# Performance work log

Hardware: AMD Instinct MI355X
Metric: run time of the kernel (lower is better)

Reference implementation:

```python
import jax, jax.numpy as jnp
import numpy as np

N = 100000
IN_C, HID_C, OUT_C = 128, 128, 128
E = 3200000


def gcn_conv(x, src, dst, W, b, num_nodes):
    # Linear transform first (smaller feature dim already), then normalized scatter-add.
    h = x @ W  # [N, out]
    # symmetric normalization with self-loops already included in (src, dst)
    deg = jax.ops.segment_sum(jnp.ones_like(dst, dtype=h.dtype), dst, num_segments=num_nodes)
    dinv = jnp.where(deg > 0, jax.lax.rsqrt(deg), 0.0)  # deg^{-1/2}
    norm = dinv[src] * dinv[dst]  # [E_total]
    msgs = h[src] * norm[:, None]  # gather + scale, [E_total, out]
    out = jax.ops.segment_sum(msgs, dst, num_segments=num_nodes)  # scatter-add
    return out + b


def add_self_loops(edge_index, num_nodes):
    loop = jnp.arange(num_nodes, dtype=edge_index.dtype)
    src = jnp.concatenate([edge_index[0], loop])
    dst = jnp.concatenate([edge_index[1], loop])
    return src, dst


def setup_inputs() -> dict:
    key = jax.random.key(0)
    k1, k2, k3, k4, k5 = jax.random.split(key, 5)
    x = jax.random.normal(k1, (N, IN_C), dtype=jnp.float32)
    edge_index = jax.random.randint(k2, (2, E), 0, N, dtype=jnp.int64)
    # Glorot-ish init for GCN weights
    W1 = jax.random.normal(k3, (IN_C, HID_C), dtype=jnp.float32) * (1.0 / np.sqrt(IN_C))
    b1 = jnp.zeros((HID_C,), dtype=jnp.float32)
    W2 = jax.random.normal(k4, (HID_C, OUT_C), dtype=jnp.float32) * (1.0 / np.sqrt(HID_C))
    b2 = jnp.zeros((OUT_C,), dtype=jnp.float32)
    return {"x": x, "edge_index": edge_index, "W1": W1, "b1": b1, "W2": W2, "b2": b2}


def reference(x, edge_index, W1, b1, W2, b2):
    src, dst = add_self_loops(edge_index, N)
    h = gcn_conv(x, src, dst, W1, b1, N)
    h = jax.nn.relu(h)
    out = gcn_conv(h, src, dst, W2, b2, N)
    return out
```

## Files before the change

### kernel.cpp

```cpp
#include <hip/hip_runtime.h>


#define NPB 128
#define NBMAX 1024
#define EPT 64
#define PART_TILE (256 * EPT)
#define CAP 5120

typedef unsigned short ushort_t;
typedef unsigned long long ull_t;
typedef __attribute__((ext_vector_type(8))) short short8;
typedef __attribute__((ext_vector_type(4))) float f32x4;

__device__ __forceinline__ unsigned short f32_to_bf16_rne(float x) {
    unsigned int v = __float_as_uint(x);
    unsigned int r = v + 0x7fffu + ((v >> 16) & 1u);
    return (unsigned short)(r >> 16);
}

__global__ __launch_bounds__(256) void k_part2(
    const int* __restrict__ src, const int* __restrict__ dst,
    int* __restrict__ cnt, unsigned int* __restrict__ pairs,
    int e, int nbp, int total) {
    __shared__ int lcnt[NBMAX];
    __shared__ int lbase[NBMAX];
    int t = threadIdx.x;
    int t0 = blockIdx.x * PART_TILE;
    for (int k = t; k < nbp; k += 256) lcnt[k] = 0;
    __syncthreads();
#pragma unroll 4
    for (int j = 0; j < EPT; j++) {
        int i = t0 + j * 256 + t;
        if (i < total) {
            int d = (i < e) ? dst[i] : (i - e);
            atomicAdd(&lcnt[d >> 7], 1);
        }
    }
    __syncthreads();
    for (int k = t; k < nbp; k += 256) {
        int c = lcnt[k];
        lbase[k] = c ? atomicAdd(&cnt[k], c) : 0;
        lcnt[k] = 0;
    }
    __syncthreads();
#pragma unroll 4
    for (int j = 0; j < EPT; j++) {
        int i = t0 + j * 256 + t;
        if (i < total) {
            int s, d;
            if (i < e) { s = src[i]; d = dst[i]; }
            else       { s = i - e;  d = s; }
            int b = d >> 7;
            int off = atomicAdd(&lcnt[b], 1) + lbase[b];
            pairs[(size_t)b * CAP + off] =
                (unsigned int)s | ((unsigned int)(d & 127) << 17);
        }
    }
}

__global__ __launch_bounds__(256) void k_bscan(
    const int* __restrict__ cnt, int* __restrict__ bucket_ptr,
    int nbp, int total,
    const float* __restrict__ W1, const float* __restrict__ W2,
    ushort_t* __restrict__ Wp1, ushort_t* __restrict__ Wp2) {
    if (blockIdx.x > 0) {
        int idx = (blockIdx.x - 1) * 256 + threadIdx.x;
        int which = idx >> 14;
        int e = idx & 16383;
        int n = e & 127, k = e >> 7;
        const float* W = which ? W2 : W1;
        ushort_t* Wp = which ? Wp2 : Wp1;
        Wp[n * 128 + k] = f32_to_bf16_rne(W[k * 128 + n]);
        return;
    }
    __shared__ int sd[256];
    int t = threadIdx.x;
    int c[4];
#pragma unroll
    for (int j = 0; j < 4; j++) {
        int k = t * 4 + j;
        c[j] = (k < nbp) ? cnt[k] : 0;
    }
    int s = c[0] + c[1] + c[2] + c[3];
    sd[t] = s;
    __syncthreads();
    for (int off = 1; off < 256; off <<= 1) {
        int v = (t >= off) ? sd[t - off] : 0;
        __syncthreads();
        sd[t] += v;
        __syncthreads();
    }
    int pre = sd[t] - s;
#pragma unroll
    for (int j = 0; j < 4; j++) {
        int k = t * 4 + j;
        if (k < nbp) bucket_ptr[k] = pre;
        pre += c[j];
    }
    if (t == 255) bucket_ptr[nbp] = total;
}

__global__ __launch_bounds__(256) void k_build(
    const unsigned int* __restrict__ pairs, const int* __restrict__ cntg,
    const int* __restrict__ bucket_ptr,
    int* __restrict__ row_ptr, int* __restrict__ srcs,
    float* __restrict__ dinv, int n) {
    __shared__ int cnt[NPB];
    __shared__ int scn[NPB];
    __shared__ int cur[NPB];
    int b = blockIdx.x;
    int t = threadIdx.x;
    int node0 = b << 7;
    int cb = cntg[b];
    int p0 = bucket_ptr[b];
    const unsigned int* bp = pairs + (size_t)b * CAP;
    if (t < NPB) cnt[t] = 0;
    __syncthreads();
    for (int i = t; i < cb; i += 256) {
        int dlow = (int)(bp[i] >> 17) & 127;
        atomicAdd(&cnt[dlow], 1);
    }
    __syncthreads();
    if (t < NPB) scn[t] = cnt[t];
    __syncthreads();
    for (int off = 1; off < NPB; off <<= 1) {
        int v = (t < NPB && t >= off) ? scn[t - off] : 0;
        __syncthreads();
        if (t < NPB) scn[t] += v;
        __syncthreads();
    }
    if (t < NPB) {
        int incl = scn[t];
        int excl = incl - cnt[t];
        int start = p0 + excl;
        cur[t] = start;
        int node = node0 + t;
        if (node < n) {
            row_ptr[node] = start;
            dinv[node] = rsqrtf((float)cnt[t]);
            if (node == n - 1) row_ptr[n] = p0 + incl;
        }
    }
    __syncthreads();
    for (int i = t; i < cb; i += 256) {
        unsigned int pr = bp[i];
        int pos = atomicAdd(&cur[(pr >> 17) & 127], 1);
        srcs[pos] = (int)(pr & 0x1FFFFu);
    }
}

__global__ __launch_bounds__(256) void k_gemm1(
    const float* __restrict__ A, const ushort_t* __restrict__ Wp,
    const float* __restrict__ dinv, ushort_t* __restrict__ G, int M) {
    int t = threadIdx.x;
    int row0 = blockIdx.x * 64;
    int wv = t >> 6;
    int lane = t & 63;
    int m = lane & 15;
    int quad = lane >> 4;

    int gr_row = row0 + wv * 16 + m;
    int gcl = gr_row < M ? gr_row : M - 1;
    const float* ap = A + (size_t)gcl * 128 + quad * 8;

    f32x4 acc[8];
#pragma unroll
    for (int c = 0; c < 8; c++) acc[c] = (f32x4){0.f, 0.f, 0.f, 0.f};

#pragma unroll
    for (int ks = 0; ks < 4; ks++) {
        int kb = ks * 32 + quad * 8;
        float xs[8];
        *(float4*)&xs[0] = *(const float4*)(ap + ks * 32);
        *(float4*)&xs[4] = *(const float4*)(ap + ks * 32 + 4);
        short8 ahi, alo;
#pragma unroll
        for (int j = 0; j < 8; j++) {
            unsigned short h = f32_to_bf16_rne(xs[j]);
            ahi[j] = (short)h;
            float hf = __uint_as_float((unsigned int)h << 16);
            alo[j] = (short)f32_to_bf16_rne(xs[j] - hf);
        }
#pragma unroll
        for (int c = 0; c < 8; c++) {
            short8 b8 = *(const short8*)(Wp + (size_t)(c * 16 + m) * 128 + kb);
            acc[c] = __builtin_amdgcn_mfma_f32_16x16x32_bf16(ahi, b8, acc[c], 0, 0, 0);
            acc[c] = __builtin_amdgcn_mfma_f32_16x16x32_bf16(alo, b8, acc[c], 0, 0, 0);
        }
    }

    int rbase = row0 + wv * 16 + quad * 4;
#pragma unroll
    for (int reg = 0; reg < 4; reg++) {
        int gr = rbase + reg;
        if (gr < M) {
            float dv = dinv[gr];
#pragma unroll
            for (int c = 0; c < 8; c++)
                G[((size_t)(c >> 2) * M + gr) * 64 + (c & 3) * 16 + m] =
                    f32_to_bf16_rne(acc[c][reg] * dv);
        }
    }
}

__global__ __launch_bounds__(256) void k_gemm2(
    ushort_t* actG2, const ushort_t* __restrict__ Wp,
    const float* __restrict__ dinv, int M) {
    int t = threadIdx.x;
    int row0 = blockIdx.x * 64;
    int wv = t >> 6;
    int lane = t & 63;
    int m = lane & 15;
    int quad = lane >> 4;

    int gr_row = row0 + wv * 16 + m;
    int gcl = gr_row < M ? gr_row : M - 1;

    f32x4 acc[8];
#pragma unroll
    for (int c = 0; c < 8; c++) acc[c] = (f32x4){0.f, 0.f, 0.f, 0.f};

#pragma unroll
    for (int ks = 0; ks < 4; ks++) {
        int kb = ks * 32 + quad * 8;
        short8 a8 = *(const short8*)(actG2 + ((size_t)(kb >> 6) * M + gcl) * 64 + (kb & 63));
#pragma unroll
        for (int c = 0; c < 8; c++) {
            short8 b8 = *(const short8*)(Wp + (size_t)(c * 16 + m) * 128 + kb);
            acc[c] = __builtin_amdgcn_mfma_f32_16x16x32_bf16(a8, b8, acc[c], 0, 0, 0);
        }
    }

    int rbase = row0 + wv * 16 + quad * 4;
#pragma unroll
    for (int reg = 0; reg < 4; reg++) {
        int gr = rbase + reg;
        if (gr < M) {
            float dv = dinv[gr];
#pragma unroll
            for (int c = 0; c < 8; c++)
                actG2[((size_t)(c >> 2) * M + gr) * 64 + (c & 3) * 16 + m] =
                    f32_to_bf16_rne(acc[c][reg] * dv);
        }
    }
}


#define ACC_U(u)                                     \
    do {                                             \
        unsigned int ul_ = (unsigned int)(u);        \
        unsigned int uh_ = (unsigned int)((u) >> 32);\
        a0 += __uint_as_float(ul_ << 16);            \
        a1 += __uint_as_float(ul_ & 0xffff0000u);    \
        a2 += __uint_as_float(uh_ << 16);            \
        a3 += __uint_as_float(uh_ & 0xffff0000u);    \
    } while (0)

__global__ __launch_bounds__(256) void k_agg1(
    const int* __restrict__ row_ptr, const int* __restrict__ srcs,
    const ushort_t* __restrict__ G, const float* __restrict__ dinv,
    const float* __restrict__ bias, ull_t* __restrict__ ActOut,
    int n) {
    int bx = blockIdx.x;
    int chunk = bx & 1;
    int tile = bx >> 1;
    int t = threadIdx.x;
    int lane = t & 63;
    int g = lane >> 4;
    int q = lane & 15;
    int node = tile * 16 + (t >> 6) * 4 + g;
    bool valid = node < n;
    int nc = valid ? node : n - 1;
    int beg = row_ptr[nc], end = row_ptr[nc + 1];
    const ull_t* Tq = (const ull_t*)G + (size_t)chunk * n * 16 + q;
    float a0 = 0.f, a1 = 0.f, a2 = 0.f, a3 = 0.f;
    int e = beg;
    for (; e + 4 <= end; e += 4) {
        int s0 = srcs[e], s1 = srcs[e + 1], s2 = srcs[e + 2], s3 = srcs[e + 3];
        ull_t u0 = Tq[(size_t)s0 * 16];
        ull_t u1 = Tq[(size_t)s1 * 16];
        ull_t u2 = Tq[(size_t)s2 * 16];
        ull_t u3 = Tq[(size_t)s3 * 16];
        ACC_U(u0); ACC_U(u1); ACC_U(u2); ACC_U(u3);
    }
    for (; e < end; ++e) {
        int s = srcs[e];
        ull_t u = Tq[(size_t)s * 16];
        ACC_U(u);
    }
    if (valid) {
        float dv = dinv[node];
        const float* bp = bias + chunk * 64 + q * 4;
        a0 = fmaxf(fmaf(a0, dv, bp[0]), 0.f);
        a1 = fmaxf(fmaf(a1, dv, bp[1]), 0.f);
        a2 = fmaxf(fmaf(a2, dv, bp[2]), 0.f);
        a3 = fmaxf(fmaf(a3, dv, bp[3]), 0.f);
        unsigned int p0 = (unsigned int)f32_to_bf16_rne(a0) |
                          ((unsigned int)f32_to_bf16_rne(a1) << 16);
        unsigned int p1 = (unsigned int)f32_to_bf16_rne(a2) |
                          ((unsigned int)f32_to_bf16_rne(a3) << 16);
        ull_t uo = (ull_t)p0 | ((ull_t)p1 << 32);
        __builtin_nontemporal_store(uo, ActOut + ((size_t)chunk * n + node) * 16 + q);
    }
}

__global__ __launch_bounds__(256) void k_agg2(
    const int* __restrict__ row_ptr, const int* __restrict__ srcs,
    const ushort_t* __restrict__ G, const float* __restrict__ dinv,
    const float* __restrict__ bias, float* __restrict__ Out,
    int n) {
    int bx = blockIdx.x;
    int chunk = bx & 1;
    int tile = bx >> 1;
    int t = threadIdx.x;
    int lane = t & 63;
    int g = lane >> 4;
    int q = lane & 15;
    int node = tile * 16 + (t >> 6) * 4 + g;
    bool valid = node < n;
    int nc = valid ? node : n - 1;
    int beg = row_ptr[nc], end = row_ptr[nc + 1];
    const ull_t* Tq = (const ull_t*)G + (size_t)chunk * n * 16 + q;
    float a0 = 0.f, a1 = 0.f, a2 = 0.f, a3 = 0.f;
    int e = beg;
    for (; e + 4 <= end; e += 4) {
        int s0 = srcs[e], s1 = srcs[e + 1], s2 = srcs[e + 2], s3 = srcs[e + 3];
        ull_t u0 = Tq[(size_t)s0 * 16];
        ull_t u1 = Tq[(size_t)s1 * 16];
        ull_t u2 = Tq[(size_t)s2 * 16];
        ull_t u3 = Tq[(size_t)s3 * 16];
        ACC_U(u0); ACC_U(u1); ACC_U(u2); ACC_U(u3);
    }
    for (; e < end; ++e) {
        int s = srcs[e];
        ull_t u = Tq[(size_t)s * 16];
        ACC_U(u);
    }
    if (valid) {
        float dv = dinv[node];
        const float* bp = bias + chunk * 64 + q * 4;
        f32x4 o;
        o.x = fmaf(a0, dv, bp[0]);
        o.y = fmaf(a1, dv, bp[1]);
        o.z = fmaf(a2, dv, bp[2]);
        o.w = fmaf(a3, dv, bp[3]);
        __builtin_nontemporal_store(o,
            (f32x4*)(Out + (size_t)node * 128 + chunk * 64 + q * 4));
    }
}

extern "C" void kernel_launch(void* const* d_in, const int* in_sizes, int n_in,
                              void* d_out, int out_size, void* d_ws, size_t ws_size,
                              hipStream_t stream) {
    const float* x  = (const float*)d_in[0];
    const int*   ei = (const int*)d_in[1];
    const float* W1 = (const float*)d_in[2];
    const float* b1 = (const float*)d_in[3];
    const float* W2 = (const float*)d_in[4];
    const float* b2 = (const float*)d_in[5];
    float* out = (float*)d_out;

    const int C = 128;
    const int N = in_sizes[0] / C;
    const int E = in_sizes[1] / 2;
    const int* src = ei;
    const int* dst = ei + E;
    const int total = E + N;
    const int nbp = (N + NPB - 1) >> 7;
    const int T = (total + PART_TILE - 1) / PART_TILE;

    char* ws = (char*)d_ws;
    size_t off = 0;
    auto alloc = [&](size_t bytes) -> void* {
        void* p = ws + off;
        off = (off + bytes + 511) & ~(size_t)511;
        return p;
    };
    int*   cnt        = (int*)alloc((size_t)nbp * 4);
    int*   bucket_ptr = (int*)alloc((size_t)(nbp + 1) * 4);
    int*   row_ptr    = (int*)alloc(((size_t)N + 1) * 4);
    float* dinv       = (float*)alloc((size_t)N * 4);
    int*   srcs       = (int*)alloc((size_t)total * 4);
    ushort_t* Wp1     = (ushort_t*)alloc(128 * 128 * 2);
    ushort_t* Wp2     = (ushort_t*)alloc(128 * 128 * 2);
    ushort_t* G1      = (ushort_t*)alloc((size_t)N * C * 2);
    size_t ab = (size_t)N * C * 2, pb = (size_t)nbp * CAP * 4;
    void* shared = alloc(ab > pb ? ab : pb);
    ushort_t* actG2 = (ushort_t*)shared;
    unsigned int* pairs = (unsigned int*)shared;

    hipMemsetAsync(cnt, 0, (size_t)nbp * 4, stream);
    k_part2<<<T, 256, 0, stream>>>(src, dst, cnt, pairs, E, nbp, total);
    k_bscan<<<129, 256, 0, stream>>>(cnt, bucket_ptr, nbp, total,
                                     W1, W2, Wp1, Wp2);
    k_build<<<nbp, 256, 0, stream>>>(pairs, cnt, bucket_ptr,
                                     row_ptr, srcs, dinv, N);

    const int half = (N + 15) / 16;
    dim3 agrid(half * 2);

    k_gemm1<<<(N + 63) / 64, 256, 0, stream>>>(x, Wp1, dinv, G1, N);
    k_agg1<<<agrid, 256, 0, stream>>>(row_ptr, srcs, G1, dinv, b1,
                                      (ull_t*)actG2, N);

    k_gemm2<<<(N + 63) / 64, 256, 0, stream>>>(actG2, Wp2, dinv, N);
    k_agg2<<<agrid, 256, 0, stream>>>(row_ptr, srcs, actG2, dinv, b2, out, N);
}
```

Before: 496.0 us.

## Drop bucket scan kernel by using padded per-bucket CSR with start/end pairs

Removes the bucket prefix-scan kernel. Each bucket's sources are now stored at a fixed CAP-strided offset, and each node keeps a packed 64-bit start/end pair in place of row_ptr. The weight transpose and bf16 conversion moves into extra blocks of the partition kernel. The partition kernel now uses smaller tiles and keeps src/dst in registers, so edges are read once instead of twice. The aggregation kernels use nontemporal loads for the index streams. In exchange, srcs becomes a padded array and the partition launches more blocks with more global atomics.

```diff
diff --git a/kernel.cpp b/kernel.cpp
--- a/kernel.cpp
+++ b/kernel.cpp
@@ -3,8 +3,8 @@
 
 #define NPB 128
 #define NBMAX 1024
-#define EPT 64
-#define PART_TILE (256 * EPT)
+#define EPT2 16
+#define PART_TILE2 (256 * EPT2)
 #define CAP 5120
 
 typedef unsigned short ushort_t;
@@ -21,19 +21,36 @@
 __global__ __launch_bounds__(256) void k_part2(
     const int* __restrict__ src, const int* __restrict__ dst,
     int* __restrict__ cnt, unsigned int* __restrict__ pairs,
-    int e, int nbp, int total) {
+    int e, int nbp, int total, int T2,
+    const float* __restrict__ W1, const float* __restrict__ W2,
+    ushort_t* __restrict__ Wp1, ushort_t* __restrict__ Wp2) {
+    int blk = blockIdx.x;
+    int t = threadIdx.x;
+    if (blk >= T2) {
+        int idx = (blk - T2) * 256 + t;
+        int which = idx >> 14;
+        int ee = idx & 16383;
+        int n = ee & 127, k = ee >> 7;
+        const float* W = which ? W2 : W1;
+        ushort_t* Wp = which ? Wp2 : Wp1;
+        Wp[n * 128 + k] = f32_to_bf16_rne(W[k * 128 + n]);
+        return;
+    }
     __shared__ int lcnt[NBMAX];
     __shared__ int lbase[NBMAX];
-    int t = threadIdx.x;
-    int t0 = blockIdx.x * PART_TILE;
+    int t0 = blk * PART_TILE2;
     for (int k = t; k < nbp; k += 256) lcnt[k] = 0;
     __syncthreads();
-#pragma unroll 4
-    for (int j = 0; j < EPT; j++) {
+    int sv[EPT2], dvv[EPT2];
+#pragma unroll
+    for (int j = 0; j < EPT2; j++) {
         int i = t0 + j * 256 + t;
         if (i < total) {
-            int d = (i < e) ? dst[i] : (i - e);
-            atomicAdd(&lcnt[d >> 7], 1);
+            if (i < e) { sv[j] = src[i]; dvv[j] = dst[i]; }
+            else       { sv[j] = i - e;  dvv[j] = sv[j]; }
+            atomicAdd(&lcnt[dvv[j] >> 7], 1);
+        } else {
+            dvv[j] = -1;
         }
     }
     __syncthreads();
@@ -43,67 +60,20 @@
         lcnt[k] = 0;
     }
     __syncthreads();
-#pragma unroll 4
-    for (int j = 0; j < EPT; j++) {
-        int i = t0 + j * 256 + t;
-        if (i < total) {
-            int s, d;
-            if (i < e) { s = src[i]; d = dst[i]; }
-            else       { s = i - e;  d = s; }
-            int b = d >> 7;
+#pragma unroll
+    for (int j = 0; j < EPT2; j++) {
+        if (dvv[j] >= 0) {
+            int b = dvv[j] >> 7;
             int off = atomicAdd(&lcnt[b], 1) + lbase[b];
             pairs[(size_t)b * CAP + off] =
-                (unsigned int)s | ((unsigned int)(d & 127) << 17);
-        }
-    }
-}
-
-__global__ __launch_bounds__(256) void k_bscan(
-    const int* __restrict__ cnt, int* __restrict__ bucket_ptr,
-    int nbp, int total,
-    const float* __restrict__ W1, const float* __restrict__ W2,
-    ushort_t* __restrict__ Wp1, ushort_t* __restrict__ Wp2) {
-    if (blockIdx.x > 0) {
-        int idx = (blockIdx.x - 1) * 256 + threadIdx.x;
-        int which = idx >> 14;
-        int e = idx & 16383;
-        int n = e & 127, k = e >> 7;
-        const float* W = which ? W2 : W1;
-        ushort_t* Wp = which ? Wp2 : Wp1;
-        Wp[n * 128 + k] = f32_to_bf16_rne(W[k * 128 + n]);
-        return;
-    }
-    __shared__ int sd[256];
-    int t = threadIdx.x;
-    int c[4];
-#pragma unroll
-    for (int j = 0; j < 4; j++) {
-        int k = t * 4 + j;
-        c[j] = (k < nbp) ? cnt[k] : 0;
-    }
-    int s = c[0] + c[1] + c[2] + c[3];
-    sd[t] = s;
-    __syncthreads();
-    for (int off = 1; off < 256; off <<= 1) {
-        int v = (t >= off) ? sd[t - off] : 0;
-        __syncthreads();
-        sd[t] += v;
-        __syncthreads();
-    }
-    int pre = sd[t] - s;
-#pragma unroll
-    for (int j = 0; j < 4; j++) {
-        int k = t * 4 + j;
-        if (k < nbp) bucket_ptr[k] = pre;
-        pre += c[j];
-    }
-    if (t == 255) bucket_ptr[nbp] = total;
+                (unsigned int)sv[j] | ((unsigned int)(dvv[j] & 127) << 17);
+        }
+    }
 }
 
 __global__ __launch_bounds__(256) void k_build(
     const unsigned int* __restrict__ pairs, const int* __restrict__ cntg,
-    const int* __restrict__ bucket_ptr,
-    int* __restrict__ row_ptr, int* __restrict__ srcs,
+    ull_t* __restrict__ row_se, int* __restrict__ srcs,
     float* __restrict__ dinv, int n) {
     __shared__ int cnt[NPB];
     __shared__ int scn[NPB];
@@ -112,8 +82,8 @@
     int t = threadIdx.x;
     int node0 = b << 7;
     int cb = cntg[b];
-    int p0 = bucket_ptr[b];
-    const unsigned int* bp = pairs + (size_t)b * CAP;
+    int base = b * CAP;
+    const unsigned int* bp = pairs + (size_t)base;
     if (t < NPB) cnt[t] = 0;
     __syncthreads();
     for (int i = t; i < cb; i += 256) {
@@ -132,20 +102,20 @@
     if (t < NPB) {
         int incl = scn[t];
         int excl = incl - cnt[t];
-        int start = p0 + excl;
-        cur[t] = start;
+        cur[t] = excl;
         int node = node0 + t;
         if (node < n) {
-            row_ptr[node] = start;
+            row_se[node] = (ull_t)(unsigned int)(base + excl) |
+                           ((ull_t)(unsigned int)(base + incl) << 32);
             dinv[node] = rsqrtf((float)cnt[t]);
-            if (node == n - 1) row_ptr[n] = p0 + incl;
-        }
-    }
-    __syncthreads();
+        }
+    }
+    __syncthreads();
+    int* bs = srcs + (size_t)base;
     for (int i = t; i < cb; i += 256) {
         unsigned int pr = bp[i];
         int pos = atomicAdd(&cur[(pr >> 17) & 127], 1);
-        srcs[pos] = (int)(pr & 0x1FFFFu);
+        bs[pos] = (int)(pr & 0x1FFFFu);
     }
 }
 
@@ -257,7 +227,7 @@
     } while (0)
 
 __global__ __launch_bounds__(256) void k_agg1(
-    const int* __restrict__ row_ptr, const int* __restrict__ srcs,
+    const ull_t* __restrict__ row_se, const int* __restrict__ srcs,
     const ushort_t* __restrict__ G, const float* __restrict__ dinv,
     const float* __restrict__ bias, ull_t* __restrict__ ActOut,
     int n) {
@@ -271,12 +241,16 @@
     int node = tile * 16 + (t >> 6) * 4 + g;
     bool valid = node < n;
     int nc = valid ? node : n - 1;
-    int beg = row_ptr[nc], end = row_ptr[nc + 1];
+    ull_t se = __builtin_nontemporal_load(&row_se[nc]);
+    int beg = (int)(unsigned int)se, end = (int)(unsigned int)(se >> 32);
     const ull_t* Tq = (const ull_t*)G + (size_t)chunk * n * 16 + q;
     float a0 = 0.f, a1 = 0.f, a2 = 0.f, a3 = 0.f;
     int e = beg;
     for (; e + 4 <= end; e += 4) {
-        int s0 = srcs[e], s1 = srcs[e + 1], s2 = srcs[e + 2], s3 = srcs[e + 3];
+        int s0 = __builtin_nontemporal_load(&srcs[e]);
+        int s1 = __builtin_nontemporal_load(&srcs[e + 1]);
+        int s2 = __builtin_nontemporal_load(&srcs[e + 2]);
+        int s3 = __builtin_nontemporal_load(&srcs[e + 3]);
         ull_t u0 = Tq[(size_t)s0 * 16];
         ull_t u1 = Tq[(size_t)s1 * 16];
         ull_t u2 = Tq[(size_t)s2 * 16];
@@ -284,7 +258,7 @@
         ACC_U(u0); ACC_U(u1); ACC_U(u2); ACC_U(u3);
     }
     for (; e < end; ++e) {
-        int s = srcs[e];
+        int s = __builtin_nontemporal_load(&srcs[e]);
         ull_t u = Tq[(size_t)s * 16];
         ACC_U(u);
     }
@@ -305,7 +279,7 @@
 }
 
 __global__ __launch_bounds__(256) void k_agg2(
-    const int* __restrict__ row_ptr, const int* __restrict__ srcs,
+    const ull_t* __restrict__ row_se, const int* __restrict__ srcs,
     const ushort_t* __restrict__ G, const float* __restrict__ dinv,
     const float* __restrict__ bias, float* __restrict__ Out,
     int n) {
@@ -319,12 +293,16 @@
     int node = tile * 16 + (t >> 6) * 4 + g;
     bool valid = node < n;
     int nc = valid ? node : n - 1;
-    int beg = row_ptr[nc], end = row_ptr[nc + 1];
+    ull_t se = __builtin_nontemporal_load(&row_se[nc]);
+    int beg = (int)(unsigned int)se, end = (int)(unsigned int)(se >> 32);
     const ull_t* Tq = (const ull_t*)G + (size_t)chunk * n * 16 + q;
     float a0 = 0.f, a1 = 0.f, a2 = 0.f, a3 = 0.f;
     int e = beg;
     for (; e + 4 <= end; e += 4) {
-        int s0 = srcs[e], s1 = srcs[e + 1], s2 = srcs[e + 2], s3 = srcs[e + 3];
+        int s0 = __builtin_nontemporal_load(&srcs[e]);
+        int s1 = __builtin_nontemporal_load(&srcs[e + 1]);
+        int s2 = __builtin_nontemporal_load(&srcs[e + 2]);
+        int s3 = __builtin_nontemporal_load(&srcs[e + 3]);
         ull_t u0 = Tq[(size_t)s0 * 16];
         ull_t u1 = Tq[(size_t)s1 * 16];
         ull_t u2 = Tq[(size_t)s2 * 16];
@@ -332,7 +310,7 @@
         ACC_U(u0); ACC_U(u1); ACC_U(u2); ACC_U(u3);
     }
     for (; e < end; ++e) {
-        int s = srcs[e];
+        int s = __builtin_nontemporal_load(&srcs[e]);
         ull_t u = Tq[(size_t)s * 16];
         ACC_U(u);
     }
@@ -367,7 +345,7 @@
     const int* dst = ei + E;
     const int total = E + N;
     const int nbp = (N + NPB - 1) >> 7;
-    const int T = (total + PART_TILE - 1) / PART_TILE;
+    const int T2 = (total + PART_TILE2 - 1) / PART_TILE2;
 
     char* ws = (char*)d_ws;
     size_t off = 0;
@@ -376,33 +354,30 @@
         off = (off + bytes + 511) & ~(size_t)511;
         return p;
     };
-    int*   cnt        = (int*)alloc((size_t)nbp * 4);
-    int*   bucket_ptr = (int*)alloc((size_t)(nbp + 1) * 4);
-    int*   row_ptr    = (int*)alloc(((size_t)N + 1) * 4);
-    float* dinv       = (float*)alloc((size_t)N * 4);
-    int*   srcs       = (int*)alloc((size_t)total * 4);
-    ushort_t* Wp1     = (ushort_t*)alloc(128 * 128 * 2);
-    ushort_t* Wp2     = (ushort_t*)alloc(128 * 128 * 2);
-    ushort_t* G1      = (ushort_t*)alloc((size_t)N * C * 2);
+    int*   cnt     = (int*)alloc((size_t)nbp * 4);
+    ull_t* row_se  = (ull_t*)alloc((size_t)N * 8);
+    float* dinv    = (float*)alloc((size_t)N * 4);
+    int*   srcs    = (int*)alloc((size_t)nbp * CAP * 4);
+    ushort_t* Wp1  = (ushort_t*)alloc(128 * 128 * 2);
+    ushort_t* Wp2  = (ushort_t*)alloc(128 * 128 * 2);
+    ushort_t* G1   = (ushort_t*)alloc((size_t)N * C * 2);
     size_t ab = (size_t)N * C * 2, pb = (size_t)nbp * CAP * 4;
     void* shared = alloc(ab > pb ? ab : pb);
     ushort_t* actG2 = (ushort_t*)shared;
     unsigned int* pairs = (unsigned int*)shared;
 
     hipMemsetAsync(cnt, 0, (size_t)nbp * 4, stream);
-    k_part2<<<T, 256, 0, stream>>>(src, dst, cnt, pairs, E, nbp, total);
-    k_bscan<<<129, 256, 0, stream>>>(cnt, bucket_ptr, nbp, total,
-                                     W1, W2, Wp1, Wp2);
-    k_build<<<nbp, 256, 0, stream>>>(pairs, cnt, bucket_ptr,
-                                     row_ptr, srcs, dinv, N);
+    k_part2<<<T2 + 128, 256, 0, stream>>>(src, dst, cnt, pairs, E, nbp, total,
+                                          T2, W1, W2, Wp1, Wp2);
+    k_build<<<nbp, 256, 0, stream>>>(pairs, cnt, row_se, srcs, dinv, N);
 
     const int half = (N + 15) / 16;
     dim3 agrid(half * 2);
 
     k_gemm1<<<(N + 63) / 64, 256, 0, stream>>>(x, Wp1, dinv, G1, N);
-    k_agg1<<<agrid, 256, 0, stream>>>(row_ptr, srcs, G1, dinv, b1,
+    k_agg1<<<agrid, 256, 0, stream>>>(row_se, srcs, G1, dinv, b1,
                                       (ull_t*)actG2, N);
 
     k_gemm2<<<(N + 63) / 64, 256, 0, stream>>>(actG2, Wp2, dinv, N);
-    k_agg2<<<agrid, 256, 0, stream>>>(row_ptr, srcs, actG2, dinv, b2, out, N);
-}
+    k_agg2<<<agrid, 256, 0, stream>>>(row_se, srcs, actG2, dinv, b2, out, N);
+}
```

Result: slower. 511.5 us (+3.1%).
